# Kernel optimization log

Measured on AMD Instinct MI355X. Metric: run time of the kernel, lower is better.

Reference implementation:

```python
import jax, jax.numpy as jnp
import numpy as np

N = 50000        # nodes
E = 800000       # edges (before self-loops)
F_IN = 256       # input feature dim
HID = 64         # hidden per head (concat=False -> head mean)
NCLS = 40        # classes
HEADS = 8
NEG_SLOPE = 0.2  # PyG GATConv default leaky_relu slope


def setup_inputs() -> dict:
    key = jax.random.key(0)
    ks = jax.random.split(key, 11)
    s = 0.1
    return {
        "x": jax.random.normal(ks[0], (N, F_IN), jnp.float32),
        "edge_index": jax.random.randint(ks[1], (2, E), 0, N, dtype=jnp.int64),
        "edge_attr": jax.random.uniform(ks[2], (E, 1), jnp.float32),
        "W0": jax.random.normal(ks[3], (HEADS * HID, F_IN), jnp.float32) * s,
        "a0s": jax.random.normal(ks[4], (HEADS, HID), jnp.float32) * s,
        "a0d": jax.random.normal(ks[5], (HEADS, HID), jnp.float32) * s,
        "b0": jnp.zeros((HID,), jnp.float32),
        "W2": jax.random.normal(ks[6], (HEADS * NCLS, HID), jnp.float32) * s,
        "a2s": jax.random.normal(ks[7], (HEADS, NCLS), jnp.float32) * s,
        "a2d": jax.random.normal(ks[8], (HEADS, NCLS), jnp.float32) * s,
        "b2": jnp.zeros((NCLS,), jnp.float32),
    }


def _gat_conv(x, src, dst, W, att_src, att_dst, bias, heads, out_c):
    # Linear: [N, in] @ [heads*out, in]^T -> [N, heads, out]
    h = (x @ W.T).reshape(N, heads, out_c)
    # Per-node attention logits, gathered per edge.
    a_s = jnp.einsum('nhc,hc->nh', h, att_src)
    a_d = jnp.einsum('nhc,hc->nh', h, att_dst)
    e = jax.nn.leaky_relu(a_s[src] + a_d[dst], NEG_SLOPE)  # [E, H]
    # Segment softmax over incoming edges of each destination node.
    m = jax.ops.segment_max(e, dst, num_segments=N)
    p = jnp.exp(e - m[dst])
    denom = jax.ops.segment_sum(p, dst, num_segments=N)
    alpha = p / (denom[dst] + 1e-16)
    # Weighted message scatter-sum: [E,H,C] -> [N,H,C]
    out = jax.ops.segment_sum(alpha[:, :, None] * h[src], dst, num_segments=N)
    # concat=False -> mean over heads, then bias.
    return out.mean(axis=1) + bias


def reference(x, edge_index, edge_attr, W0, a0s, a0d, b0, W2, a2s, a2d, b2):
    # edge_attr is unpacked by the torch forward but never used by GATConv.
    # PyG GATConv adds self-loops by default.
    loops = jnp.arange(N, dtype=edge_index.dtype)
    src = jnp.concatenate([edge_index[0], loops])
    dst = jnp.concatenate([edge_index[1], loops])
    h = jax.nn.relu(_gat_conv(x, src, dst, W0, a0s, a0d, b0, HEADS, HID))
    # dropout is identity in eval mode
    out = _gat_conv(h, src, dst, W2, a2s, a2d, b2, HEADS, NCLS)
    return jax.nn.log_softmax(out, axis=1)
```

## Files before the change

kernel.cpp:

```cpp
#include <hip/hip_runtime.h>
#include <hip/hip_bf16.h>
#include <math.h>


#define NEG_SLOPE 0.2f

typedef short v8s __attribute__((ext_vector_type(8)));
typedef float v4f __attribute__((ext_vector_type(4)));
typedef float v2f __attribute__((ext_vector_type(2)));
typedef unsigned short u16;
typedef unsigned int u32;
typedef unsigned char u8;

__device__ __forceinline__ u16 f2bf(float f) {
    union { float f; u32 u; } v; v.f = f;
    u32 r = v.u + 0x7fffu + ((v.u >> 16) & 1u);
    return (u16)(r >> 16);
}
__device__ __forceinline__ float lrelu_exp(float e) {
    e = (e > 0.f) ? e : NEG_SLOPE * e;
    return __expf(e);
}
__device__ __forceinline__ void dec8(uint2 r, float* h) {
    v2f a = __builtin_amdgcn_cvt_pk_f32_fp8(r.x, false);
    v2f b = __builtin_amdgcn_cvt_pk_f32_fp8(r.x, true);
    v2f c = __builtin_amdgcn_cvt_pk_f32_fp8(r.y, false);
    v2f d = __builtin_amdgcn_cvt_pk_f32_fp8(r.y, true);
    h[0] = a.x; h[1] = a.y; h[2] = b.x; h[3] = b.y;
    h[4] = c.x; h[5] = c.y; h[6] = d.x; h[7] = d.y;
}
__device__ __forceinline__ u8 enc8(float v) {
    u32 p = __builtin_amdgcn_cvt_pk_fp8_f32(v, v, 0u, false);
    return (u8)(p & 0xffu);
}


__global__ __launch_bounds__(256) void hist_k(const int* __restrict__ ei, int* __restrict__ deg,
                                              int E, int Nn) {
    int e = blockIdx.x * 256 + threadIdx.x;
    int ET = E + Nn;
    if (e >= ET) return;
    int d = (e < E) ? ei[E + e] : (e - E);
    atomicAdd(&deg[d], 1);
}

__global__ __launch_bounds__(1024) void scanA_k(const int* __restrict__ deg, int* __restrict__ incl,
                                                int* __restrict__ bsum, int n) {
    __shared__ int wsum[16];
    int t = threadIdx.x;
    int i = blockIdx.x * 1024 + t;
    int v = (i < n) ? deg[i] : 0;
    int lane = t & 63, wid = t >> 6;
    int sv = v;
    for (int off = 1; off < 64; off <<= 1) {
        int u = __shfl_up(sv, off, 64);
        if (lane >= off) sv += u;
    }
    if (lane == 63) wsum[wid] = sv;
    __syncthreads();
    if (t < 16) {
        int w = wsum[t];
        for (int off = 1; off < 16; off <<= 1) {
            int u = __shfl_up(w, off, 64);
            if (t >= off) w += u;
        }
        wsum[t] = w;
    }
    __syncthreads();
    int pre = (wid > 0) ? wsum[wid - 1] : 0;
    int inc = pre + sv;
    if (i < n) incl[i] = inc;
    if (t == 1023) bsum[blockIdx.x] = inc;
}

__global__ __launch_bounds__(64) void scanB_k(const int* __restrict__ bsum, int* __restrict__ boff, int B) {
    int t = threadIdx.x;
    int v = (t < B) ? bsum[t] : 0;
    int sv = v;
    for (int off = 1; off < 64; off <<= 1) {
        int u = __shfl_up(sv, off, 64);
        if (t >= off) sv += u;
    }
    if (t < B) boff[t] = sv - v;
    if (t == 63) boff[B] = sv;
}

__global__ __launch_bounds__(256) void scanC_k(const int* __restrict__ incl, const int* __restrict__ deg,
                                               const int* __restrict__ boff, int* __restrict__ rowstart,
                                               int n, int B) {
    int i = blockIdx.x * 256 + threadIdx.x;
    if (i < n) rowstart[i] = boff[i >> 10] + incl[i] - deg[i];
    if (i == 0) rowstart[n] = boff[B];
}

__global__ __launch_bounds__(256) void scatter_k(const int* __restrict__ ei,
                                                 const int* __restrict__ rowstart,
                                                 int* __restrict__ cursor,
                                                 int* __restrict__ srcs, int E, int Nn) {
    int e = blockIdx.x * 256 + threadIdx.x;
    int ET = E + Nn;
    if (e >= ET) return;
    int s, d;
    if (e < E) { s = ei[e]; d = ei[E + e]; }
    else       { s = e - E; d = e - E; }
    int pos = atomicAdd(&cursor[d], 1);
    srcs[rowstart[d] + pos] = s;
}


__global__ __launch_bounds__(256) void cast_k(const float* __restrict__ in, u16* __restrict__ out, int n) {
    int i = (blockIdx.x * 256 + threadIdx.x) * 4;
    if (i + 3 < n) {
        float4 v = *reinterpret_cast<const float4*>(in + i);
        ushort4 o;
        o.x = f2bf(v.x); o.y = f2bf(v.y); o.z = f2bf(v.z); o.w = f2bf(v.w);
        *reinterpret_cast<ushort4*>(out + i) = o;
    } else {
        for (int j = i; j < n; j++) out[j] = f2bf(in[j]);
    }
}


__global__ __launch_bounds__(256) void gemm_mfma(const u16* __restrict__ Ab,
                                                 const float* __restrict__ Bf,
                                                 u8* __restrict__ Cf, int M, int Nc, int K,
                                                 const float* __restrict__ avs_vec,
                                                 const float* __restrict__ avd_vec,
                                                 float* as_out, float* ad_out) {
    __shared__ __align__(16) u8 lds[20480];
    u16 (*As)[40] = reinterpret_cast<u16(*)[40]>(lds);
    u16 (*Bs)[40] = reinterpret_cast<u16(*)[40]>(lds + 10240);
    const int t = threadIdx.x;
    const int m0 = blockIdx.x * 128;
    const int n0 = blockIdx.y * 128;
    const int w = t >> 6, lane = t & 63;
    const int wr = (w >> 1) * 64, wc = (w & 1) * 64;
    const int q = lane >> 4, l16 = lane & 15;
    const int r0 = t >> 2;
    const int c8 = (t & 3) * 8;

    v4f acc[4][4];
#pragma unroll
    for (int i = 0; i < 4; i++)
#pragma unroll
        for (int j = 0; j < 4; j++) acc[i][j] = (v4f){0.f, 0.f, 0.f, 0.f};

    for (int kt = 0; kt < K; kt += 32) {
#pragma unroll
        for (int p = 0; p < 2; p++) {
            int r = r0 + p * 64;
            int gm = m0 + r;
            uint4 va = make_uint4(0u, 0u, 0u, 0u);
            if (gm < M) va = *reinterpret_cast<const uint4*>(Ab + (size_t)gm * K + kt + c8);
            *reinterpret_cast<uint4*>(&As[r][c8]) = va;
            int gn = n0 + r;
            u16 b8[8] = {0, 0, 0, 0, 0, 0, 0, 0};
            if (gn < Nc) {
                float4 w0 = *reinterpret_cast<const float4*>(Bf + (size_t)gn * K + kt + c8);
                float4 w1 = *reinterpret_cast<const float4*>(Bf + (size_t)gn * K + kt + c8 + 4);
                b8[0] = f2bf(w0.x); b8[1] = f2bf(w0.y); b8[2] = f2bf(w0.z); b8[3] = f2bf(w0.w);
                b8[4] = f2bf(w1.x); b8[5] = f2bf(w1.y); b8[6] = f2bf(w1.z); b8[7] = f2bf(w1.w);
            }
            *reinterpret_cast<uint4*>(&Bs[r][c8]) = *reinterpret_cast<const uint4*>(b8);
        }
        __syncthreads();
        v8s af[4], bf[4];
#pragma unroll
        for (int i = 0; i < 4; i++) af[i] = *reinterpret_cast<const v8s*>(&As[wr + i * 16 + l16][q * 8]);
#pragma unroll
        for (int j = 0; j < 4; j++) bf[j] = *reinterpret_cast<const v8s*>(&Bs[wc + j * 16 + l16][q * 8]);
#pragma unroll
        for (int i = 0; i < 4; i++)
#pragma unroll
            for (int j = 0; j < 4; j++)
                acc[i][j] = __builtin_amdgcn_mfma_f32_16x16x32_bf16(af[i], bf[j], acc[i][j], 0, 0, 0);
        __syncthreads();
    }

    const bool do_att = (as_out != nullptr);
    float avs[4], avd[4];
    if (do_att) {
#pragma unroll
        for (int j = 0; j < 4; j++) {
            int gn = n0 + wc + j * 16 + l16;
            avs[j] = (gn < Nc) ? avs_vec[gn] : 0.f;
            avd[j] = (gn < Nc) ? avd_vec[gn] : 0.f;
        }
    }
    const int head = (n0 + wc) >> 6;

    u8* Cs = lds;
#pragma unroll
    for (int i = 0; i < 4; i++) {
#pragma unroll
        for (int r = 0; r < 4; r++) {
            int row = wr + i * 16 + q * 4 + r;
#pragma unroll
            for (int j = 0; j < 4; j++)
                Cs[row * 144 + wc + j * 16 + l16] = enc8(acc[i][j][r]);
            if (do_att) {
                int gm = m0 + row;
                float ps = 0.f, pd = 0.f;
#pragma unroll
                for (int j = 0; j < 4; j++) {
                    float v = acc[i][j][r];
                    ps = fmaf(v, avs[j], ps);
                    pd = fmaf(v, avd[j], pd);
                }
#pragma unroll
                for (int m = 1; m < 16; m <<= 1) {
                    ps += __shfl_xor(ps, m, 64);
                    pd += __shfl_xor(pd, m, 64);
                }
                if (l16 == 0 && gm < M) {
                    as_out[gm * 8 + head] = ps;
                    ad_out[gm * 8 + head] = pd;
                }
            }
        }
    }
    __syncthreads();
#pragma unroll
    for (int it = 0; it < 4; it++) {
        int idx = it * 256 + t;
        int row = idx >> 3, ch = idx & 7;
        int gm = m0 + row, gn = n0 + ch * 16;
        if (gm < M && gn < Nc)
            *reinterpret_cast<uint4*>(Cf + (size_t)gm * Nc + gn) =
                *reinterpret_cast<const uint4*>(&Cs[row * 144 + ch * 16]);
    }
}


__global__ __launch_bounds__(256) void agg1_k(const u8* __restrict__ h1f,
                                              const float* __restrict__ as1, const float* __restrict__ ad1,
                                              const int* __restrict__ srcs, const int* __restrict__ rowstart,
                                              const float* __restrict__ b0, u16* __restrict__ x1b, int Nn) {
    int wave = threadIdx.x >> 6, lane = threadIdx.x & 63;
    int n = blockIdx.x * 4 + wave;
    if (n >= Nn) return;
    const int hl = lane >> 3;
    const float adl = ad1[n * 8 + hl];
    const size_t loff = (size_t)lane * 8;
    float acc[8] = {0, 0, 0, 0, 0, 0, 0, 0};
    float dsum = 0.f;
    int beg = rowstart[n], end = rowstart[n + 1];
    int i = beg;
    for (; i + 8 <= end; i += 8) {
        int s[8];
#pragma unroll
        for (int u = 0; u < 8; u++) s[u] = srcs[i + u];
        uint2 rw[8];
#pragma unroll
        for (int u = 0; u < 8; u++) rw[u] = *reinterpret_cast<const uint2*>(h1f + (size_t)s[u] * 512 + loff);
        float eg[8];
#pragma unroll
        for (int u = 0; u < 8; u++) eg[u] = as1[s[u] * 8 + hl];
        float p[8];
#pragma unroll
        for (int u = 0; u < 8; u++) { p[u] = lrelu_exp(eg[u] + adl); dsum += p[u]; }
#pragma unroll
        for (int u = 0; u < 8; u++) {
            float hv[8];
            dec8(rw[u], hv);
#pragma unroll
            for (int j = 0; j < 8; j++) acc[j] = fmaf(p[u], hv[j], acc[j]);
        }
    }
    for (; i + 4 <= end; i += 4) {
        int s[4];
#pragma unroll
        for (int u = 0; u < 4; u++) s[u] = srcs[i + u];
        uint2 rw[4];
#pragma unroll
        for (int u = 0; u < 4; u++) rw[u] = *reinterpret_cast<const uint2*>(h1f + (size_t)s[u] * 512 + loff);
#pragma unroll
        for (int u = 0; u < 4; u++) {
            float p = lrelu_exp(as1[s[u] * 8 + hl] + adl);
            dsum += p;
            float hv[8];
            dec8(rw[u], hv);
#pragma unroll
            for (int j = 0; j < 8; j++) acc[j] = fmaf(p, hv[j], acc[j]);
        }
    }
    for (; i < end; i++) {
        int s = srcs[i];
        uint2 raw = *reinterpret_cast<const uint2*>(h1f + (size_t)s * 512 + loff);
        float p = lrelu_exp(as1[s * 8 + hl] + adl);
        dsum += p;
        float hv[8];
        dec8(raw, hv);
#pragma unroll
        for (int j = 0; j < 8; j++) acc[j] = fmaf(p, hv[j], acc[j]);
    }
    float inv = 1.f / (dsum + 1e-16f);
    float r[8];
#pragma unroll
    for (int j = 0; j < 8; j++) r[j] = acc[j] * inv;
#pragma unroll
    for (int j = 0; j < 8; j++) {
        r[j] += __shfl_xor(r[j], 8, 64);
        r[j] += __shfl_xor(r[j], 16, 64);
        r[j] += __shfl_xor(r[j], 32, 64);
    }
    if (lane < 8) {
        u16 o[8];
#pragma unroll
        for (int j = 0; j < 8; j++) {
            float v = r[j] * 0.125f + b0[lane * 8 + j];
            o[j] = f2bf((v > 0.f) ? v : 0.f);
        }
        *reinterpret_cast<uint4*>(x1b + (size_t)n * 64 + lane * 8) =
            *reinterpret_cast<const uint4*>(o);
    }
}


__global__ __launch_bounds__(256) void att2_k(const u8* __restrict__ h2f,
                                              const float* __restrict__ a2s, const float* __restrict__ a2d,
                                              float* __restrict__ as2, float* __restrict__ ad2, int Nn) {
    int t = blockIdx.x * 256 + threadIdx.x;
    if (t >= Nn * 8) return;
    int n = t >> 3, h = t & 7;
    const u8* hr = h2f + (size_t)n * 320 + h * 40;
    float s1 = 0.f, s2 = 0.f;
#pragma unroll
    for (int b = 0; b < 5; b++) {
        uint2 raw = *reinterpret_cast<const uint2*>(hr + b * 8);
        float h8[8];
        dec8(raw, h8);
#pragma unroll
        for (int j = 0; j < 8; j++) {
            int c = h * 40 + b * 8 + j;
            s1 = fmaf(h8[j], a2s[c], s1);
            s2 = fmaf(h8[j], a2d[c], s2);
        }
    }
    as2[t] = s1;
    ad2[t] = s2;
}


__global__ __launch_bounds__(256) void agg2_k(const u8* __restrict__ h2f,
                                              const float* __restrict__ as2, const float* __restrict__ ad2,
                                              const int* __restrict__ srcs, const int* __restrict__ rowstart,
                                              const float* __restrict__ b2, float* __restrict__ out, int Nn) {
    __shared__ float smem[4][320];
    int wave = threadIdx.x >> 6, lane = threadIdx.x & 63;
    int n = blockIdx.x * 4 + wave;
    bool active = (n < Nn);
    bool ld = active && (lane < 40);
    const int hl = lane / 5;
    float adl = ld ? ad2[n * 8 + hl] : 0.f;
    float acc[8] = {0, 0, 0, 0, 0, 0, 0, 0};
    float dsum = 0.f;
    if (ld) {
        const size_t loff = (size_t)lane * 8;
        int beg = rowstart[n], end = rowstart[n + 1];
        int i = beg;
        for (; i + 8 <= end; i += 8) {
            int s[8];
#pragma unroll
            for (int u = 0; u < 8; u++) s[u] = srcs[i + u];
            uint2 rw[8];
#pragma unroll
            for (int u = 0; u < 8; u++) rw[u] = *reinterpret_cast<const uint2*>(h2f + (size_t)s[u] * 320 + loff);
            float eg[8];
#pragma unroll
            for (int u = 0; u < 8; u++) eg[u] = as2[s[u] * 8 + hl];
            float p[8];
#pragma unroll
            for (int u = 0; u < 8; u++) { p[u] = lrelu_exp(eg[u] + adl); dsum += p[u]; }
#pragma unroll
            for (int u = 0; u < 8; u++) {
                float hv[8];
                dec8(rw[u], hv);
#pragma unroll
                for (int j = 0; j < 8; j++) acc[j] = fmaf(p[u], hv[j], acc[j]);
            }
        }
        for (; i + 4 <= end; i += 4) {
            int s[4];
#pragma unroll
            for (int u = 0; u < 4; u++) s[u] = srcs[i + u];
            uint2 rw[4];
#pragma unroll
            for (int u = 0; u < 4; u++) rw[u] = *reinterpret_cast<const uint2*>(h2f + (size_t)s[u] * 320 + loff);
#pragma unroll
            for (int u = 0; u < 4; u++) {
                float p = lrelu_exp(as2[s[u] * 8 + hl] + adl);
                dsum += p;
                float hv[8];
                dec8(rw[u], hv);
#pragma unroll
                for (int j = 0; j < 8; j++) acc[j] = fmaf(p, hv[j], acc[j]);
            }
        }
        for (; i < end; i++) {
            int s = srcs[i];
            uint2 raw = *reinterpret_cast<const uint2*>(h2f + (size_t)s * 320 + loff);
            float p = lrelu_exp(as2[s * 8 + hl] + adl);
            dsum += p;
            float hv[8];
            dec8(raw, hv);
#pragma unroll
            for (int j = 0; j < 8; j++) acc[j] = fmaf(p, hv[j], acc[j]);
        }
        float inv = 1.f / (dsum + 1e-16f);
#pragma unroll
        for (int j = 0; j < 8; j++) smem[wave][lane * 8 + j] = acc[j] * inv;
    }
    __syncthreads();
    if (active) {
        float v;
        if (lane < 40) {
            float ssum = 0.f;
#pragma unroll
            for (int h = 0; h < 8; h++) ssum += smem[wave][h * 40 + lane];
            v = ssum * 0.125f + b2[lane];
        } else {
            v = -INFINITY;
        }
        float m = v;
        for (int off = 32; off > 0; off >>= 1) m = fmaxf(m, __shfl_xor(m, off, 64));
        float ex = (lane < 40) ? __expf(v - m) : 0.f;
        float se = ex;
        for (int off = 32; off > 0; off >>= 1) se += __shfl_xor(se, off, 64);
        if (lane < 40) out[(size_t)n * 40 + lane] = v - m - __logf(se);
    }
}


extern "C" void kernel_launch(void* const* d_in, const int* in_sizes, int n_in,
                              void* d_out, int out_size, void* d_ws, size_t ws_size,
                              hipStream_t stream) {
    const float* x   = (const float*)d_in[0];
    const int*   ei  = (const int*)d_in[1];
    const float* W0  = (const float*)d_in[3];
    const float* a0s = (const float*)d_in[4];
    const float* a0d = (const float*)d_in[5];
    const float* b0  = (const float*)d_in[6];
    const float* W2  = (const float*)d_in[7];
    const float* a2s = (const float*)d_in[8];
    const float* a2d = (const float*)d_in[9];
    const float* b2  = (const float*)d_in[10];
    float* out = (float*)d_out;

    const int Nn = in_sizes[0] / 256;
    const int E  = in_sizes[1] / 2;
    const int ET = E + Nn;
    const int NB = (Nn + 1023) / 1024;

    size_t off = 0;
    auto carve = [&](size_t bytes) -> void* {
        void* p = (char*)d_ws + off;
        off += (bytes + 255) & ~(size_t)255;
        return p;
    };
    u16*   xb       = (u16*)carve((size_t)Nn * 256 * 2);
    u8*    h1f      = (u8*)carve((size_t)Nn * 512);
    u16*   x1b      = (u16*)carve((size_t)Nn * 64 * 2);
    u8*    h2f      = (u8*)carve((size_t)Nn * 320);
    float* as1      = (float*)carve((size_t)Nn * 8 * 4);
    float* ad1      = (float*)carve((size_t)Nn * 8 * 4);
    float* as2      = (float*)carve((size_t)Nn * 8 * 4);
    float* ad2      = (float*)carve((size_t)Nn * 8 * 4);
    int*   deg      = (int*)carve((size_t)Nn * 4);
    int*   cursor   = (int*)carve((size_t)Nn * 4);
    int*   rowstart = (int*)carve((size_t)(Nn + 1) * 4);
    int*   srcs     = (int*)carve((size_t)ET * 4);
    int*   incl     = (int*)carve((size_t)Nn * 4);
    int*   bsum     = (int*)carve(64 * 4);
    int*   boff     = (int*)carve(65 * 4);

    hipMemsetAsync(deg, 0, (size_t)Nn * 4, stream);
    hipMemsetAsync(cursor, 0, (size_t)Nn * 4, stream);

    hist_k<<<(ET + 255) / 256, 256, 0, stream>>>(ei, deg, E, Nn);
    scanA_k<<<NB, 1024, 0, stream>>>(deg, incl, bsum, Nn);
    scanB_k<<<1, 64, 0, stream>>>(bsum, boff, NB);
    scanC_k<<<(Nn + 255) / 256, 256, 0, stream>>>(incl, deg, boff, rowstart, Nn, NB);
    scatter_k<<<(ET + 255) / 256, 256, 0, stream>>>(ei, rowstart, cursor, srcs, E, Nn);

    cast_k<<<(Nn * 256 / 4 + 255) / 256, 256, 0, stream>>>(x, xb, Nn * 256);

    gemm_mfma<<<dim3((Nn + 127) / 128, 4), 256, 0, stream>>>(
        xb, W0, h1f, Nn, 512, 256, a0s, a0d, as1, ad1);
    agg1_k<<<(Nn + 3) / 4, 256, 0, stream>>>(h1f, as1, ad1, srcs, rowstart, b0, x1b, Nn);

    gemm_mfma<<<dim3((Nn + 127) / 128, 3), 256, 0, stream>>>(
        x1b, W2, h2f, Nn, 320, 64, nullptr, nullptr, nullptr, nullptr);
    att2_k<<<(Nn * 8 + 255) / 256, 256, 0, stream>>>(h2f, a2s, a2d, as2, ad2, Nn);
    agg2_k<<<(Nn + 3) / 4, 256, 0, stream>>>(h2f, as2, ad2, srcs, rowstart, b2, out, Nn);
}
```

Before: 417.5 us.

## Retile MFMA GEMM to 128x64 with K=64 steps and pre-cast bf16 weights

The GEMM tile changes from 128x128 with a K step of 32 to 128x64 with a K step of 64, so each of the four waves now owns a 32x64 sub-tile. The weights are cast to bf16 once by separate kernels, which removes the per-tile fp32 loads and conversions inside the GEMM. Launch bounds now ask for 4 blocks per CU to raise occupancy. In exchange, the A tile is reloaded twice as often across the N dimension, and two small cast launches are added. Narrower N tiles also fix the attention head at one per block, which the layer-2 padding of 320 = 5x64 relies on.

```diff
diff --git a/kernel.cpp b/kernel.cpp
--- a/kernel.cpp
+++ b/kernel.cpp
@@ -121,59 +121,61 @@
 }
 
 
-__global__ __launch_bounds__(256) void gemm_mfma(const u16* __restrict__ Ab,
-                                                 const float* __restrict__ Bf,
-                                                 u8* __restrict__ Cf, int M, int Nc, int K,
-                                                 const float* __restrict__ avs_vec,
-                                                 const float* __restrict__ avd_vec,
-                                                 float* as_out, float* ad_out) {
-    __shared__ __align__(16) u8 lds[20480];
-    u16 (*As)[40] = reinterpret_cast<u16(*)[40]>(lds);
-    u16 (*Bs)[40] = reinterpret_cast<u16(*)[40]>(lds + 10240);
+__global__ __launch_bounds__(256, 4) void gemm_mfma(const u16* __restrict__ Ab,
+                                                    const u16* __restrict__ Bb,
+                                                    u8* __restrict__ Cf, int M, int Nc, int K,
+                                                    const float* __restrict__ avs_vec,
+                                                    const float* __restrict__ avd_vec,
+                                                    float* as_out, float* ad_out) {
+    __shared__ __align__(16) u8 lds[27648];
+    u16 (*As)[72] = reinterpret_cast<u16(*)[72]>(lds);
+    u16 (*Bs)[72] = reinterpret_cast<u16(*)[72]>(lds + 18432);
     const int t = threadIdx.x;
     const int m0 = blockIdx.x * 128;
-    const int n0 = blockIdx.y * 128;
+    const int n0 = blockIdx.y * 64;
     const int w = t >> 6, lane = t & 63;
-    const int wr = (w >> 1) * 64, wc = (w & 1) * 64;
+    const int wr = w * 32;
     const int q = lane >> 4, l16 = lane & 15;
-    const int r0 = t >> 2;
-    const int c8 = (t & 3) * 8;
-
-    v4f acc[4][4];
-#pragma unroll
-    for (int i = 0; i < 4; i++)
+
+    v4f acc[2][4];
+#pragma unroll
+    for (int i = 0; i < 2; i++)
 #pragma unroll
         for (int j = 0; j < 4; j++) acc[i][j] = (v4f){0.f, 0.f, 0.f, 0.f};
 
-    for (int kt = 0; kt < K; kt += 32) {
-#pragma unroll
-        for (int p = 0; p < 2; p++) {
-            int r = r0 + p * 64;
-            int gm = m0 + r;
+    for (int kt = 0; kt < K; kt += 64) {
+#pragma unroll
+        for (int it = 0; it < 4; it++) {
+            int c = it * 256 + t;
+            int row = c >> 3, col8 = (c & 7) * 8;
+            int gm = m0 + row;
             uint4 va = make_uint4(0u, 0u, 0u, 0u);
-            if (gm < M) va = *reinterpret_cast<const uint4*>(Ab + (size_t)gm * K + kt + c8);
-            *reinterpret_cast<uint4*>(&As[r][c8]) = va;
-            int gn = n0 + r;
-            u16 b8[8] = {0, 0, 0, 0, 0, 0, 0, 0};
-            if (gn < Nc) {
-                float4 w0 = *reinterpret_cast<const float4*>(Bf + (size_t)gn * K + kt + c8);
-                float4 w1 = *reinterpret_cast<const float4*>(Bf + (size_t)gn * K + kt + c8 + 4);
-                b8[0] = f2bf(w0.x); b8[1] = f2bf(w0.y); b8[2] = f2bf(w0.z); b8[3] = f2bf(w0.w);
-                b8[4] = f2bf(w1.x); b8[5] = f2bf(w1.y); b8[6] = f2bf(w1.z); b8[7] = f2bf(w1.w);
-            }
-            *reinterpret_cast<uint4*>(&Bs[r][c8]) = *reinterpret_cast<const uint4*>(b8);
+            if (gm < M) va = *reinterpret_cast<const uint4*>(Ab + (size_t)gm * K + kt + col8);
+            *reinterpret_cast<uint4*>(&As[row][col8]) = va;
+        }
+#pragma unroll
+        for (int it = 0; it < 2; it++) {
+            int c = it * 256 + t;
+            int row = c >> 3, col8 = (c & 7) * 8;
+            uint4 vb = *reinterpret_cast<const uint4*>(Bb + (size_t)(n0 + row) * K + kt + col8);
+            *reinterpret_cast<uint4*>(&Bs[row][col8]) = vb;
         }
         __syncthreads();
-        v8s af[4], bf[4];
-#pragma unroll
-        for (int i = 0; i < 4; i++) af[i] = *reinterpret_cast<const v8s*>(&As[wr + i * 16 + l16][q * 8]);
-#pragma unroll
-        for (int j = 0; j < 4; j++) bf[j] = *reinterpret_cast<const v8s*>(&Bs[wc + j * 16 + l16][q * 8]);
-#pragma unroll
-        for (int i = 0; i < 4; i++)
+#pragma unroll
+        for (int ks = 0; ks < 2; ks++) {
+            v8s af[2], bf[4];
+#pragma unroll
+            for (int i = 0; i < 2; i++)
+                af[i] = *reinterpret_cast<const v8s*>(&As[wr + i * 16 + l16][ks * 32 + q * 8]);
 #pragma unroll
             for (int j = 0; j < 4; j++)
-                acc[i][j] = __builtin_amdgcn_mfma_f32_16x16x32_bf16(af[i], bf[j], acc[i][j], 0, 0, 0);
+                bf[j] = *reinterpret_cast<const v8s*>(&Bs[j * 16 + l16][ks * 32 + q * 8]);
+#pragma unroll
+            for (int i = 0; i < 2; i++)
+#pragma unroll
+                for (int j = 0; j < 4; j++)
+                    acc[i][j] = __builtin_amdgcn_mfma_f32_16x16x32_bf16(af[i], bf[j], acc[i][j], 0, 0, 0);
+        }
         __syncthreads();
     }
 
@@ -182,22 +184,21 @@
     if (do_att) {
 #pragma unroll
         for (int j = 0; j < 4; j++) {
-            int gn = n0 + wc + j * 16 + l16;
-            avs[j] = (gn < Nc) ? avs_vec[gn] : 0.f;
-            avd[j] = (gn < Nc) ? avd_vec[gn] : 0.f;
-        }
-    }
-    const int head = (n0 + wc) >> 6;
+            avs[j] = avs_vec[n0 + j * 16 + l16];
+            avd[j] = avd_vec[n0 + j * 16 + l16];
+        }
+    }
+    const int head = n0 >> 6;
 
     u8* Cs = lds;
 #pragma unroll
-    for (int i = 0; i < 4; i++) {
+    for (int i = 0; i < 2; i++) {
 #pragma unroll
         for (int r = 0; r < 4; r++) {
             int row = wr + i * 16 + q * 4 + r;
 #pragma unroll
             for (int j = 0; j < 4; j++)
-                Cs[row * 144 + wc + j * 16 + l16] = enc8(acc[i][j][r]);
+                Cs[row * 80 + j * 16 + l16] = enc8(acc[i][j][r]);
             if (do_att) {
                 int gm = m0 + row;
                 float ps = 0.f, pd = 0.f;
@@ -221,13 +222,13 @@
     }
     __syncthreads();
 #pragma unroll
-    for (int it = 0; it < 4; it++) {
+    for (int it = 0; it < 2; it++) {
         int idx = it * 256 + t;
-        int row = idx >> 3, ch = idx & 7;
-        int gm = m0 + row, gn = n0 + ch * 16;
-        if (gm < M && gn < Nc)
-            *reinterpret_cast<uint4*>(Cf + (size_t)gm * Nc + gn) =
-                *reinterpret_cast<const uint4*>(&Cs[row * 144 + ch * 16]);
+        int row = idx >> 2, ch = idx & 3;
+        int gm = m0 + row;
+        if (gm < M)
+            *reinterpret_cast<uint4*>(Cf + (size_t)gm * Nc + n0 + ch * 16) =
+                *reinterpret_cast<const uint4*>(&Cs[row * 80 + ch * 16]);
     }
 }
 
@@ -459,6 +460,8 @@
         return p;
     };
     u16*   xb       = (u16*)carve((size_t)Nn * 256 * 2);
+    u16*   W0b      = (u16*)carve((size_t)512 * 256 * 2);
+    u16*   W2b      = (u16*)carve((size_t)320 * 64 * 2);
     u8*    h1f      = (u8*)carve((size_t)Nn * 512);
     u16*   x1b      = (u16*)carve((size_t)Nn * 64 * 2);
     u8*    h2f      = (u8*)carve((size_t)Nn * 320);
@@ -484,13 +487,15 @@
     scatter_k<<<(ET + 255) / 256, 256, 0, stream>>>(ei, rowstart, cursor, srcs, E, Nn);
 
     cast_k<<<(Nn * 256 / 4 + 255) / 256, 256, 0, stream>>>(x, xb, Nn * 256);
-
-    gemm_mfma<<<dim3((Nn + 127) / 128, 4), 256, 0, stream>>>(
-        xb, W0, h1f, Nn, 512, 256, a0s, a0d, as1, ad1);
+    cast_k<<<(512 * 256 / 4 + 255) / 256, 256, 0, stream>>>(W0, W0b, 512 * 256);
+    cast_k<<<(320 * 64 / 4 + 255) / 256, 256, 0, stream>>>(W2, W2b, 320 * 64);
+
+    gemm_mfma<<<dim3((Nn + 127) / 128, 8), 256, 0, stream>>>(
+        xb, W0b, h1f, Nn, 512, 256, a0s, a0d, as1, ad1);
     agg1_k<<<(Nn + 3) / 4, 256, 0, stream>>>(h1f, as1, ad1, srcs, rowstart, b0, x1b, Nn);
 
-    gemm_mfma<<<dim3((Nn + 127) / 128, 3), 256, 0, stream>>>(
-        x1b, W2, h2f, Nn, 320, 64, nullptr, nullptr, nullptr, nullptr);
+    gemm_mfma<<<dim3((Nn + 127) / 128, 5), 256, 0, stream>>>(
+        x1b, W2b, h2f, Nn, 320, 64, nullptr, nullptr, nullptr, nullptr);
     att2_k<<<(Nn * 8 + 255) / 256, 256, 0, stream>>>(h2f, a2s, a2d, as2, ad2, Nn);
     agg2_k<<<(Nn + 3) / 4, 256, 0, stream>>>(h2f, as2, ad2, srcs, rowstart, b2, out, Nn);
 }
```

Result: faster. 404.3 us (-3.2%).
